# Optimization experiments

Hardware: AMD Instinct MI355X
Metric: run time of the kernel (lower is better)

Reference implementation:

```python
import jax, jax.numpy as jnp
import numpy as np

N, C, K = 200000, 128, 27  # active voxels, channels, 3x3x3 kernel taps
EPS = 1e-5  # torch LayerNorm default


def setup_inputs() -> dict:
    key = jax.random.key(0)
    ks = jax.random.split(key, 8)
    feats = jax.random.normal(ks[0], (N, C), dtype=jnp.float32)
    # plan-based gather map: neighbor row index per voxel per kernel tap
    neighbor_idx = jax.random.randint(ks[1], (N, K), 0, N, dtype=jnp.int32)
    # sparse conv weights: one [C_in, C_out] slice per kernel offset
    conv_w = jax.random.normal(ks[2], (K, C, C), dtype=jnp.float32) * (1.0 / np.sqrt(K * C))
    conv_b = jax.random.normal(ks[3], (C,), dtype=jnp.float32) * 0.02
    # torch.nn.Linear(C, C): weight [out, in], y = x @ W^T + b
    lin_w = jax.random.normal(ks[4], (C, C), dtype=jnp.float32) * (1.0 / np.sqrt(C))
    lin_b = jax.random.normal(ks[5], (C,), dtype=jnp.float32) * 0.02
    ln_w = 1.0 + 0.02 * jax.random.normal(ks[6], (C,), dtype=jnp.float32)
    ln_b = 0.02 * jax.random.normal(ks[7], (C,), dtype=jnp.float32)
    return {
        "feats": feats, "neighbor_idx": neighbor_idx,
        "conv_w": conv_w, "conv_b": conv_b,
        "lin_w": lin_w, "lin_b": lin_b,
        "ln_w": ln_w, "ln_b": ln_b,
    }


def _sparse_conv(feats, neighbor_idx, conv_w, conv_b):
    # Stream over the 27 kernel taps: gather [N,C] then GEMM with the tap's
    # [C,C] slice; never materialize the [N,27,C] gathered tensor.
    def step(acc, tap):
        idx_k, w_k = tap  # idx_k: [N], w_k: [C, C]
        return acc + feats[idx_k] @ w_k, None

    acc0 = jnp.zeros((feats.shape[0], conv_w.shape[2]), dtype=feats.dtype)
    out, _ = jax.lax.scan(step, acc0, (neighbor_idx.T, conv_w))
    return out + conv_b


def reference(feats, neighbor_idx, conv_w, conv_b, lin_w, lin_b, ln_w, ln_b):
    x = _sparse_conv(feats, neighbor_idx, conv_w, conv_b)   # [N, C]
    x = x @ lin_w.T + lin_b                                  # Linear
    mu = jnp.mean(x, axis=-1, keepdims=True)                 # LayerNorm
    var = jnp.mean(jnp.square(x - mu), axis=-1, keepdims=True)
    x = (x - mu) * jax.lax.rsqrt(var + EPS) * ln_w + ln_b
    return x
```

## Files before the change

### kernel.cpp

```cpp
#include <hip/hip_runtime.h>
#include <hip/hip_bf16.h>
#include <stdint.h>

#define N_ROWS 200000
#define C_DIM  128
#define TAPS   27
#define EPS    1e-5f

typedef __attribute__((ext_vector_type(8)))  short  short8;
typedef __attribute__((ext_vector_type(16))) float  floatx16;

__device__ __forceinline__ unsigned int f2bf(float f) {
  union { float f; unsigned int u; } v; v.f = f;
  unsigned int r = v.u + 0x7FFFu + ((v.u >> 16) & 1u);
  return r >> 16;
}

__device__ __forceinline__ void glds16(const unsigned short* g, unsigned short* l) {
  __builtin_amdgcn_global_load_lds(
      (const __attribute__((address_space(1))) unsigned int*)g,
      (__attribute__((address_space(3))) unsigned int*)l, 16, 0, 0);
}

__global__ __launch_bounds__(256) void k_cast(const float* __restrict__ in,
                                              unsigned short* __restrict__ out, int n8) {
  int i = blockIdx.x * 256 + threadIdx.x;
  if (i >= n8) return;
  const float4* p = (const float4*)in + (size_t)i * 2;
  float4 a = p[0], b = p[1];
  uint4 v;
  v.x = f2bf(a.x) | (f2bf(a.y) << 16);
  v.y = f2bf(a.z) | (f2bf(a.w) << 16);
  v.z = f2bf(b.x) | (f2bf(b.y) << 16);
  v.w = f2bf(b.z) | (f2bf(b.w) << 16);
  *(uint4*)(out + (size_t)i * 8) = v;
}

__global__ __launch_bounds__(256) void k_fold(const float* __restrict__ conv_w,
                                              const float* __restrict__ lin_w,
                                              const float* __restrict__ conv_b,
                                              const float* __restrict__ lin_b,
                                              unsigned short* __restrict__ wfrag,
                                              float* __restrict__ biasf) {
  __shared__ float lwT[128 * 128];
  for (int e = threadIdx.x; e < 16384; e += 256) {
    int co = e >> 7, t = e & 127;
    lwT[t * 128 + (co ^ (t & 31))] = lin_w[e];
  }
  __syncthreads();

  int id = blockIdx.x * 256 + threadIdx.x;
  const int NW = TAPS * 4 * 8 * 64;
  if (id < NW) {
    int l  = id & 63;
    int s  = (id >> 6) & 7;
    int nt = (id >> 9) & 3;
    int k  = id >> 11;
    int ci0 = s * 16 + (l >> 5) * 8;
    int co  = nt * 32 + (l & 31);
    const float* cw = conv_w + ((size_t)(k * 128 + ci0)) * 128;
    float acc[8] = {0, 0, 0, 0, 0, 0, 0, 0};
    for (int t = 0; t < 128; ++t) {
      float lv = lwT[t * 128 + (co ^ (t & 31))];
#pragma unroll
      for (int j = 0; j < 8; ++j) acc[j] += cw[j * 128 + t] * lv;
    }
    uint4 v;
    v.x = f2bf(acc[0]) | (f2bf(acc[1]) << 16);
    v.y = f2bf(acc[2]) | (f2bf(acc[3]) << 16);
    v.z = f2bf(acc[4]) | (f2bf(acc[5]) << 16);
    v.w = f2bf(acc[6]) | (f2bf(acc[7]) << 16);
    *(uint4*)(wfrag + (size_t)id * 8) = v;
  } else if (id < NW + 128) {
    int co = id - NW;
    float s = lin_b[co];
    for (int t = 0; t < 128; ++t) s += conv_b[t] * lwT[t * 128 + (co ^ (t & 31))];
    biasf[co] = s;
  }
}

__global__ __launch_bounds__(512, 4) void k_main(const unsigned short* __restrict__ featsB,
                                                 const int* __restrict__ nidx,
                                                 const unsigned short* __restrict__ wfrag,
                                                 const float* __restrict__ biasf,
                                                 const float* __restrict__ lnw,
                                                 const float* __restrict__ lnb,
                                                 float* __restrict__ out) {
  __shared__ unsigned short ldsB[2][16384];

  const int tid = threadIdx.x;
  const int l   = tid & 63;
  const int w   = tid >> 6;
  const int l31 = l & 31;
  const int lh  = l >> 5;
  const int row0w = blockIdx.x * 256 + w * 32;
  const int gr  = row0w + l31;
  const int grc = (gr < N_ROWS) ? gr : 0;
  const int* np = nidx + (size_t)grc * TAPS;

  floatx16 acc0 = {0.f}, acc1 = {0.f}, acc2 = {0.f}, acc3 = {0.f};

  {
    const unsigned short* src = wfrag + (size_t)tid * 8;
    unsigned short* dst = &ldsB[0][w * 512];
#pragma unroll
    for (int r = 0; r < 4; ++r) glds16(src + r * 4096, dst + r * 4096);
  }
  int nid = np[0];

  for (int k = 0; k < TAPS; ++k) {
    const int cur = k & 1;
    if (k + 1 < TAPS) {
      const unsigned short* src = wfrag + (size_t)(k + 1) * 16384 + (size_t)tid * 8;
      unsigned short* dst = &ldsB[cur ^ 1][w * 512];
#pragma unroll
      for (int r = 0; r < 4; ++r) glds16(src + r * 4096, dst + r * 4096);
      __builtin_amdgcn_s_waitcnt(0xF74);
    } else {
      __builtin_amdgcn_s_waitcnt(0xF70);
    }
    __builtin_amdgcn_s_barrier();

    const short8* ap = (const short8*)(featsB + (size_t)(unsigned)nid * 128 + lh * 8);
    short8 a0 = ap[0],  a1 = ap[2],  a2 = ap[4],  a3 = ap[6];
    short8 a4 = ap[8],  a5 = ap[10], a6 = ap[12], a7 = ap[14];
    int nid_next = (k + 1 < TAPS) ? np[k + 1] : 0;

    const unsigned short* bb = &ldsB[cur][l * 8];
#pragma unroll
    for (int s = 0; s < 8; ++s) {
      short8 av = (s == 0) ? a0 : (s == 1) ? a1 : (s == 2) ? a2 : (s == 3) ? a3
                : (s == 4) ? a4 : (s == 5) ? a5 : (s == 6) ? a6 : a7;
      short8 b0 = *(const short8*)(bb + (0 * 8 + s) * 512);
      short8 b1 = *(const short8*)(bb + (1 * 8 + s) * 512);
      short8 b2 = *(const short8*)(bb + (2 * 8 + s) * 512);
      short8 b3 = *(const short8*)(bb + (3 * 8 + s) * 512);
      acc0 = __builtin_amdgcn_mfma_f32_32x32x16_bf16(av, b0, acc0, 0, 0, 0);
      acc1 = __builtin_amdgcn_mfma_f32_32x32x16_bf16(av, b1, acc1, 0, 0, 0);
      acc2 = __builtin_amdgcn_mfma_f32_32x32x16_bf16(av, b2, acc2, 0, 0, 0);
      acc3 = __builtin_amdgcn_mfma_f32_32x32x16_bf16(av, b3, acc3, 0, 0, 0);
    }
    __builtin_amdgcn_s_barrier();
    nid = nid_next;
  }

  float b0 = biasf[l31], b1 = biasf[32 + l31], b2 = biasf[64 + l31], b3 = biasf[96 + l31];
  float g0 = lnw[l31],   g1 = lnw[32 + l31],   g2 = lnw[64 + l31],   g3 = lnw[96 + l31];
  float c0 = lnb[l31],   c1 = lnb[32 + l31],   c2 = lnb[64 + l31],   c3 = lnb[96 + l31];

#pragma unroll
  for (int r = 0; r < 16; ++r) {
    float x0 = acc0[r] + b0, x1 = acc1[r] + b1, x2 = acc2[r] + b2, x3 = acc3[r] + b3;
    float s = x0 + x1 + x2 + x3;
    float q = x0 * x0 + x1 * x1 + x2 * x2 + x3 * x3;
#pragma unroll
    for (int off = 16; off >= 1; off >>= 1) {
      s += __shfl_xor(s, off, 64);
      q += __shfl_xor(q, off, 64);
    }
    float mu  = s * (1.0f / 128.0f);
    float var = q * (1.0f / 128.0f) - mu * mu;
    float rs  = rsqrtf(var + EPS);
    int row   = (r & 3) + 8 * (r >> 2) + 4 * lh;
    int grow  = row0w + row;
    if (grow < N_ROWS) {
      float* o = out + (size_t)grow * 128;
      o[l31]      = (x0 - mu) * rs * g0 + c0;
      o[32 + l31] = (x1 - mu) * rs * g1 + c1;
      o[64 + l31] = (x2 - mu) * rs * g2 + c2;
      o[96 + l31] = (x3 - mu) * rs * g3 + c3;
    }
  }
}

extern "C" void kernel_launch(void* const* d_in, const int* in_sizes, int n_in,
                              void* d_out, int out_size, void* d_ws, size_t ws_size,
                              hipStream_t stream) {
  const float* feats  = (const float*)d_in[0];
  const int*   nidx   = (const int*)d_in[1];
  const float* conv_w = (const float*)d_in[2];
  const float* conv_b = (const float*)d_in[3];
  const float* lin_w  = (const float*)d_in[4];
  const float* lin_b  = (const float*)d_in[5];
  const float* ln_w   = (const float*)d_in[6];
  const float* ln_b   = (const float*)d_in[7];
  float* out = (float*)d_out;

  unsigned short* featsB = (unsigned short*)d_ws;
  unsigned short* wfrag  = (unsigned short*)((char*)d_ws + 51200000);
  float*          biasf  = (float*)((char*)d_ws + 51200000 + 884736);

  int n8 = N_ROWS * C_DIM / 8;
  k_cast<<<(n8 + 255) / 256, 256, 0, stream>>>(feats, featsB, n8);
  k_fold<<<(TAPS * 2048 + 128 + 255) / 256, 256, 0, stream>>>(conv_w, lin_w, conv_b, lin_b,
                                                              wfrag, biasf);
  k_main<<<(N_ROWS + 255) / 256, 512, 0, stream>>>(featsB, nidx, wfrag, biasf, ln_w, ln_b, out);
}
```

Baseline: 504.1 us.

## Give each wave 64 rows, software-pipeline feature gathers, simplify weight folding

The main kernel now runs 4 waves of 256 threads, each owning 64 rows as two 32-row MFMA fragments. This halves the LDS weight reads per MFMA and doubles the work per barrier. The gathered feature rows for tap k+1 are loaded inside the MFMA loop of tap k, so gather latency overlaps compute, at the cost of more registers (two fragments of A operands plus eight accumulators) and lower occupancy. The fold kernel drops its 64 KB shared transpose of lin_w and reads rows with float4 directly, which should cut its launch overhead and shared-memory limits.

```diff
diff --git a/kernel.cpp b/kernel.cpp
--- a/kernel.cpp
+++ b/kernel.cpp
@@ -42,13 +42,6 @@
                                               const float* __restrict__ lin_b,
                                               unsigned short* __restrict__ wfrag,
                                               float* __restrict__ biasf) {
-  __shared__ float lwT[128 * 128];
-  for (int e = threadIdx.x; e < 16384; e += 256) {
-    int co = e >> 7, t = e & 127;
-    lwT[t * 128 + (co ^ (t & 31))] = lin_w[e];
-  }
-  __syncthreads();
-
   int id = blockIdx.x * 256 + threadIdx.x;
   const int NW = TAPS * 4 * 8 * 64;
   if (id < NW) {
@@ -58,12 +51,16 @@
     int k  = id >> 11;
     int ci0 = s * 16 + (l >> 5) * 8;
     int co  = nt * 32 + (l & 31);
-    const float* cw = conv_w + ((size_t)(k * 128 + ci0)) * 128;
+    const float4* lw4 = (const float4*)(lin_w + (size_t)co * 128);
+    const float4* cw4 = (const float4*)(conv_w + ((size_t)(k * 128 + ci0)) * 128);
     float acc[8] = {0, 0, 0, 0, 0, 0, 0, 0};
-    for (int t = 0; t < 128; ++t) {
-      float lv = lwT[t * 128 + (co ^ (t & 31))];
-#pragma unroll
-      for (int j = 0; j < 8; ++j) acc[j] += cw[j * 128 + t] * lv;
+    for (int t4 = 0; t4 < 32; ++t4) {
+      float4 lv = lw4[t4];
+#pragma unroll
+      for (int j = 0; j < 8; ++j) {
+        float4 cv = cw4[j * 32 + t4];
+        acc[j] += cv.x * lv.x + cv.y * lv.y + cv.z * lv.z + cv.w * lv.w;
+      }
     }
     uint4 v;
     v.x = f2bf(acc[0]) | (f2bf(acc[1]) << 16);
@@ -73,13 +70,14 @@
     *(uint4*)(wfrag + (size_t)id * 8) = v;
   } else if (id < NW + 128) {
     int co = id - NW;
+    const float* lw = lin_w + (size_t)co * 128;
     float s = lin_b[co];
-    for (int t = 0; t < 128; ++t) s += conv_b[t] * lwT[t * 128 + (co ^ (t & 31))];
+    for (int t = 0; t < 128; ++t) s += conv_b[t] * lw[t];
     biasf[co] = s;
   }
 }
 
-__global__ __launch_bounds__(512, 4) void k_main(const unsigned short* __restrict__ featsB,
+__global__ __launch_bounds__(256, 2) void k_main(const unsigned short* __restrict__ featsB,
                                                  const int* __restrict__ nidx,
                                                  const unsigned short* __restrict__ wfrag,
                                                  const float* __restrict__ biasf,
@@ -93,82 +91,105 @@
   const int w   = tid >> 6;
   const int l31 = l & 31;
   const int lh  = l >> 5;
-  const int row0w = blockIdx.x * 256 + w * 32;
-  const int gr  = row0w + l31;
-  const int grc = (gr < N_ROWS) ? gr : 0;
-  const int* np = nidx + (size_t)grc * TAPS;
-
-  floatx16 acc0 = {0.f}, acc1 = {0.f}, acc2 = {0.f}, acc3 = {0.f};
-
+  const int row0w = blockIdx.x * 256 + w * 64;
+
+  const int gr0 = row0w + l31;
+  const int gr1 = gr0 + 32;
+  const int gc0 = (gr0 < N_ROWS) ? gr0 : N_ROWS - 1;
+  const int gc1 = (gr1 < N_ROWS) ? gr1 : N_ROWS - 1;
+  const int* np0 = nidx + (size_t)gc0 * TAPS;
+  const int* np1 = nidx + (size_t)gc1 * TAPS;
+
+  floatx16 acc[2][4];
+#pragma unroll
+  for (int rf = 0; rf < 2; ++rf)
+#pragma unroll
+    for (int c = 0; c < 4; ++c) acc[rf][c] = (floatx16){0.f};
+
+#pragma unroll
+  for (int r = 0; r < 8; ++r)
+    glds16(wfrag + (size_t)r * 2048 + tid * 8, &ldsB[0][r * 2048 + w * 512]);
+  int nidA0 = np0[0];
+  int nidA1 = np1[0];
+  short8 a0[8], a1[8];
   {
-    const unsigned short* src = wfrag + (size_t)tid * 8;
-    unsigned short* dst = &ldsB[0][w * 512];
-#pragma unroll
-    for (int r = 0; r < 4; ++r) glds16(src + r * 4096, dst + r * 4096);
-  }
-  int nid = np[0];
+    const unsigned short* p0 = featsB + (size_t)(unsigned)nidA0 * 128 + lh * 8;
+    const unsigned short* p1 = featsB + (size_t)(unsigned)nidA1 * 128 + lh * 8;
+#pragma unroll
+    for (int s = 0; s < 8; ++s) { a0[s] = *(const short8*)(p0 + s * 16);
+                                  a1[s] = *(const short8*)(p1 + s * 16); }
+  }
+  int nidN0 = np0[1];
+  int nidN1 = np1[1];
 
   for (int k = 0; k < TAPS; ++k) {
     const int cur = k & 1;
-    if (k + 1 < TAPS) {
-      const unsigned short* src = wfrag + (size_t)(k + 1) * 16384 + (size_t)tid * 8;
+    __builtin_amdgcn_s_waitcnt(0x4F72);
+    __builtin_amdgcn_s_barrier();
+
+    const int kc1 = (k + 1 < TAPS) ? k + 1 : TAPS - 1;
+    {
+      const unsigned short* src = wfrag + (size_t)kc1 * 16384 + tid * 8;
       unsigned short* dst = &ldsB[cur ^ 1][w * 512];
 #pragma unroll
-      for (int r = 0; r < 4; ++r) glds16(src + r * 4096, dst + r * 4096);
-      __builtin_amdgcn_s_waitcnt(0xF74);
-    } else {
-      __builtin_amdgcn_s_waitcnt(0xF70);
-    }
-    __builtin_amdgcn_s_barrier();
-
-    const short8* ap = (const short8*)(featsB + (size_t)(unsigned)nid * 128 + lh * 8);
-    short8 a0 = ap[0],  a1 = ap[2],  a2 = ap[4],  a3 = ap[6];
-    short8 a4 = ap[8],  a5 = ap[10], a6 = ap[12], a7 = ap[14];
-    int nid_next = (k + 1 < TAPS) ? np[k + 1] : 0;
+      for (int r = 0; r < 8; ++r) glds16(src + r * 2048, dst + r * 2048);
+    }
+
+    const unsigned short* q0 = featsB + (size_t)(unsigned)nidN0 * 128 + lh * 8;
+    const unsigned short* q1 = featsB + (size_t)(unsigned)nidN1 * 128 + lh * 8;
 
     const unsigned short* bb = &ldsB[cur][l * 8];
 #pragma unroll
     for (int s = 0; s < 8; ++s) {
-      short8 av = (s == 0) ? a0 : (s == 1) ? a1 : (s == 2) ? a2 : (s == 3) ? a3
-                : (s == 4) ? a4 : (s == 5) ? a5 : (s == 6) ? a6 : a7;
       short8 b0 = *(const short8*)(bb + (0 * 8 + s) * 512);
       short8 b1 = *(const short8*)(bb + (1 * 8 + s) * 512);
       short8 b2 = *(const short8*)(bb + (2 * 8 + s) * 512);
       short8 b3 = *(const short8*)(bb + (3 * 8 + s) * 512);
-      acc0 = __builtin_amdgcn_mfma_f32_32x32x16_bf16(av, b0, acc0, 0, 0, 0);
-      acc1 = __builtin_amdgcn_mfma_f32_32x32x16_bf16(av, b1, acc1, 0, 0, 0);
-      acc2 = __builtin_amdgcn_mfma_f32_32x32x16_bf16(av, b2, acc2, 0, 0, 0);
-      acc3 = __builtin_amdgcn_mfma_f32_32x32x16_bf16(av, b3, acc3, 0, 0, 0);
-    }
-    __builtin_amdgcn_s_barrier();
-    nid = nid_next;
-  }
-
-  float b0 = biasf[l31], b1 = biasf[32 + l31], b2 = biasf[64 + l31], b3 = biasf[96 + l31];
-  float g0 = lnw[l31],   g1 = lnw[32 + l31],   g2 = lnw[64 + l31],   g3 = lnw[96 + l31];
-  float c0 = lnb[l31],   c1 = lnb[32 + l31],   c2 = lnb[64 + l31],   c3 = lnb[96 + l31];
-
-#pragma unroll
-  for (int r = 0; r < 16; ++r) {
-    float x0 = acc0[r] + b0, x1 = acc1[r] + b1, x2 = acc2[r] + b2, x3 = acc3[r] + b3;
-    float s = x0 + x1 + x2 + x3;
-    float q = x0 * x0 + x1 * x1 + x2 * x2 + x3 * x3;
-#pragma unroll
-    for (int off = 16; off >= 1; off >>= 1) {
-      s += __shfl_xor(s, off, 64);
-      q += __shfl_xor(q, off, 64);
-    }
-    float mu  = s * (1.0f / 128.0f);
-    float var = q * (1.0f / 128.0f) - mu * mu;
-    float rs  = rsqrtf(var + EPS);
-    int row   = (r & 3) + 8 * (r >> 2) + 4 * lh;
-    int grow  = row0w + row;
-    if (grow < N_ROWS) {
-      float* o = out + (size_t)grow * 128;
-      o[l31]      = (x0 - mu) * rs * g0 + c0;
-      o[32 + l31] = (x1 - mu) * rs * g1 + c1;
-      o[64 + l31] = (x2 - mu) * rs * g2 + c2;
-      o[96 + l31] = (x3 - mu) * rs * g3 + c3;
+      acc[0][0] = __builtin_amdgcn_mfma_f32_32x32x16_bf16(a0[s], b0, acc[0][0], 0, 0, 0);
+      acc[0][1] = __builtin_amdgcn_mfma_f32_32x32x16_bf16(a0[s], b1, acc[0][1], 0, 0, 0);
+      acc[0][2] = __builtin_amdgcn_mfma_f32_32x32x16_bf16(a0[s], b2, acc[0][2], 0, 0, 0);
+      acc[0][3] = __builtin_amdgcn_mfma_f32_32x32x16_bf16(a0[s], b3, acc[0][3], 0, 0, 0);
+      acc[1][0] = __builtin_amdgcn_mfma_f32_32x32x16_bf16(a1[s], b0, acc[1][0], 0, 0, 0);
+      acc[1][1] = __builtin_amdgcn_mfma_f32_32x32x16_bf16(a1[s], b1, acc[1][1], 0, 0, 0);
+      acc[1][2] = __builtin_amdgcn_mfma_f32_32x32x16_bf16(a1[s], b2, acc[1][2], 0, 0, 0);
+      acc[1][3] = __builtin_amdgcn_mfma_f32_32x32x16_bf16(a1[s], b3, acc[1][3], 0, 0, 0);
+      a0[s] = *(const short8*)(q0 + s * 16);
+      a1[s] = *(const short8*)(q1 + s * 16);
+    }
+    const int kc2 = (k + 2 < TAPS) ? k + 2 : TAPS - 1;
+    nidN0 = np0[kc2];
+    nidN1 = np1[kc2];
+  }
+
+  float bb0 = biasf[l31], bb1 = biasf[32 + l31], bb2 = biasf[64 + l31], bb3 = biasf[96 + l31];
+  float g0 = lnw[l31],    g1 = lnw[32 + l31],    g2 = lnw[64 + l31],    g3 = lnw[96 + l31];
+  float c0 = lnb[l31],    c1 = lnb[32 + l31],    c2 = lnb[64 + l31],    c3 = lnb[96 + l31];
+
+#pragma unroll
+  for (int rf = 0; rf < 2; ++rf) {
+#pragma unroll
+    for (int r = 0; r < 16; ++r) {
+      float x0 = acc[rf][0][r] + bb0, x1 = acc[rf][1][r] + bb1;
+      float x2 = acc[rf][2][r] + bb2, x3 = acc[rf][3][r] + bb3;
+      float s = x0 + x1 + x2 + x3;
+      float q = x0 * x0 + x1 * x1 + x2 * x2 + x3 * x3;
+#pragma unroll
+      for (int off = 16; off >= 1; off >>= 1) {
+        s += __shfl_xor(s, off, 64);
+        q += __shfl_xor(q, off, 64);
+      }
+      float mu  = s * (1.0f / 128.0f);
+      float var = q * (1.0f / 128.0f) - mu * mu;
+      float rs  = rsqrtf(var + EPS);
+      int row   = rf * 32 + (r & 3) + 8 * (r >> 2) + 4 * lh;
+      int grow  = row0w + row;
+      if (grow < N_ROWS) {
+        float* o = out + (size_t)grow * 128;
+        o[l31]      = (x0 - mu) * rs * g0 + c0;
+        o[32 + l31] = (x1 - mu) * rs * g1 + c1;
+        o[64 + l31] = (x2 - mu) * rs * g2 + c2;
+        o[96 + l31] = (x3 - mu) * rs * g3 + c3;
+      }
     }
   }
 }
@@ -194,5 +215,5 @@
   k_cast<<<(n8 + 255) / 256, 256, 0, stream>>>(feats, featsB, n8);
   k_fold<<<(TAPS * 2048 + 128 + 255) / 256, 256, 0, stream>>>(conv_w, lin_w, conv_b, lin_b,
                                                               wfrag, biasf);
-  k_main<<<(N_ROWS + 255) / 256, 512, 0, stream>>>(featsB, nidx, wfrag, biasf, ln_w, ln_b, out);
-}
+  k_main<<<(N_ROWS + 255) / 256, 256, 0, stream>>>(featsB, nidx, wfrag, biasf, ln_w, ln_b, out);
+}
```

Result: slower. 552.0 us (+9.5%).
